# Performance work log

Measured on AMD Instinct MI355X. Metric: run time of the kernel, lower is better.

The kernel has to match this reference:

```python
import jax, jax.numpy as jnp
import numpy as np

C = 256
C8 = C // 8
B, H, W = 4, 64, 64


def setup_inputs() -> dict:
    key = jax.random.key(0)
    ks = jax.random.split(key, 10)
    s = lambda fan_in: 1.0 / np.sqrt(fan_in)
    return {
        "x": jax.random.normal(ks[0], (B, C, H, W), dtype=jnp.float32),
        "conv_w": jax.random.normal(ks[1], (C8, C), dtype=jnp.float32) * s(C),
        "conv_b": jax.random.normal(ks[2], (C8,), dtype=jnp.float32) * 0.01,
        "q_w": jax.random.normal(ks[3], (C8, C8), dtype=jnp.float32) * s(C8),
        "q_b": jax.random.normal(ks[4], (C8,), dtype=jnp.float32) * 0.01,
        "k_w": jax.random.normal(ks[5], (C8, C8), dtype=jnp.float32) * s(C8),
        "k_b": jax.random.normal(ks[6], (C8,), dtype=jnp.float32) * 0.01,
        "v_w": jax.random.normal(ks[7], (C, C8), dtype=jnp.float32) * s(C8),
        "v_b": jax.random.normal(ks[8], (C,), dtype=jnp.float32) * 0.01,
        "gamma": jax.random.normal(ks[9], (1,), dtype=jnp.float32) * 0.1,
    }


def reference(x, conv_w, conv_b, q_w, q_b, k_w, k_b, v_w, v_b, gamma):
    b, c, h, w = x.shape
    hw = h * w
    # 1x1 convs are channel-mixing matmuls over flattened spatial dims
    xf = x.reshape(b, c, hw)                                   # [B, C, HW]
    proj = jnp.einsum('dc,bcn->bdn', conv_w, xf) + conv_b[None, :, None]   # [B, C8, HW]
    q = jnp.einsum('ed,bdn->bne', q_w, proj) + q_b[None, None, :]          # [B, HW, C8]
    k = jnp.einsum('ed,bdn->ben', k_w, proj) + k_b[None, :, None]          # [B, C8, HW]
    v = jnp.einsum('cd,bdn->bcn', v_w, proj) + v_b[None, :, None]          # [B, C, HW]
    attn = jax.nn.softmax(jnp.einsum('bne,bem->bnm', q, k), axis=-1)       # [B, HW, HW]
    out = jnp.einsum('bcm,bnm->bcn', v, attn)                              # [B, C, HW]
    out = out.reshape(b, c, h, w)
    return gamma[0] * out + x
```

## Files before the change

### kernel.cpp

```cpp
#include <hip/hip_runtime.h>
#include <hip/hip_bf16.h>
#include <stdint.h>

#define B_   4
#define C_   256
#define C8_  32
#define HW_  4096
#define ROWS_ 320
#define MS_  4
#define L2E  1.4426950408889634f

typedef __attribute__((ext_vector_type(8)))  short  short8;
typedef __attribute__((ext_vector_type(8)))  ushort us8;
typedef __attribute__((ext_vector_type(16))) float  f32x16;

#define WT_OFF    0
#define BALL_OFF  (256*320*4)
#define Q_OFF     (BALL_OFF + 1280)
#define KT_OFF    (Q_OFF  + B_*HW_*C8_*2)
#define V_OFF     (KT_OFF + B_*HW_*C8_*2)
#define PACC_OFF  (V_OFF  + B_*C_*HW_*2)
#define LPART_OFF (PACC_OFF + (size_t)MS_*B_*C_*HW_*2)

__device__ __forceinline__ ushort f2bf(float f) {
    union { float f; uint32_t u; } v; v.f = f;
    uint32_t u = v.u;
    uint32_t r = u + 0x7fffu + ((u >> 16) & 1u);
    return (ushort)(r >> 16);
}
__device__ __forceinline__ uint32_t pktr(float lo, float hi) {
    union { float f; uint32_t u; } a, b; a.f = lo; b.f = hi;
    return __builtin_amdgcn_perm(b.u, a.u, 0x07060302u);
}

__global__ __launch_bounds__(256) void k_setup(
    const float* __restrict__ conv_w, const float* __restrict__ conv_b,
    const float* __restrict__ q_w, const float* __restrict__ q_b,
    const float* __restrict__ k_w, const float* __restrict__ k_b,
    const float* __restrict__ v_w, const float* __restrict__ v_b,
    ushort* __restrict__ wbf, float* __restrict__ ball)
{
    int r = blockIdx.x;
    int c = threadIdx.x;
    const float* wrow;
    float bias;
    if (r < 32)       { wrow = q_w + r*32;      bias = q_b[r];      }
    else if (r < 64)  { wrow = k_w + (r-32)*32; bias = k_b[r-32];   }
    else              { wrow = v_w + (r-64)*32; bias = v_b[r-64];   }
    float acc = 0.f;
    #pragma unroll
    for (int d = 0; d < 32; ++d) acc += wrow[d] * conv_w[d*C_ + c];
    float scale = (r < 32) ? L2E : 1.0f;
    wbf[r*C_ + c] = f2bf(acc * scale);
    if (c == 0) {
        float bb = bias;
        #pragma unroll
        for (int d = 0; d < 32; ++d) bb += wrow[d] * conv_b[d];
        ball[r] = bb * scale;
    }
}

__global__ __launch_bounds__(320) void k_qkv(
    const float* __restrict__ x, const ushort* __restrict__ wbf,
    const float* __restrict__ ball,
    ushort* __restrict__ qg, ushort* __restrict__ ktg, ushort* __restrict__ vg)
{
    int blk = blockIdx.x;
    int b  = blk >> 6;
    int n0 = (blk & 63) * 64;
    int t = threadIdx.x;
    int w = t >> 6, lane = t & 63;
    int l31 = lane & 31, h = lane >> 5;

    f32x16 acc[2][2];
    #pragma unroll
    for (int i = 0; i < 2; ++i)
        #pragma unroll
        for (int j = 0; j < 2; ++j)
            acc[i][j] = (f32x16)(0.f);

    const float* xb = x + (size_t)b*C_*HW_;
    const ushort* wrow0 = wbf + (size_t)(w*64 + l31)*C_ + h*8;
    const ushort* wrow1 = wrow0 + 32*C_;

    #pragma unroll 2
    for (int kc = 0; kc < 16; ++kc) {
        int k0 = kc*16;
        short8 a0 = *(const short8*)(wrow0 + k0);
        short8 a1 = *(const short8*)(wrow1 + k0);
        #pragma unroll
        for (int ni = 0; ni < 2; ++ni) {
            const float* xc = xb + (size_t)(k0 + h*8)*HW_ + n0 + ni*32 + l31;
            union { uint32_t d[4]; short8 s8; } bf;
            #pragma unroll
            for (int j2 = 0; j2 < 4; ++j2) {
                float f0 = xc[(size_t)(2*j2    )*HW_];
                float f1 = xc[(size_t)(2*j2 + 1)*HW_];
                bf.d[j2] = pktr(f0, f1);
            }
            acc[0][ni] = __builtin_amdgcn_mfma_f32_32x32x16_bf16(a0, bf.s8, acc[0][ni], 0, 0, 0);
            acc[1][ni] = __builtin_amdgcn_mfma_f32_32x32x16_bf16(a1, bf.s8, acc[1][ni], 0, 0, 0);
        }
    }

    #pragma unroll
    for (int mi = 0; mi < 2; ++mi) {
        int rowb = w*64 + mi*32;
        #pragma unroll
        for (int ni = 0; ni < 2; ++ni) {
            int n = n0 + ni*32 + l31;
            #pragma unroll
            for (int r = 0; r < 16; ++r) {
                int row = rowb + (r & 3) + 8*(r >> 2) + 4*h;
                float v = acc[mi][ni][r] + ball[row];
                ushort bv = f2bf(v);
                if (row < 32) {
                    qg[((size_t)b*HW_ + n)*C8_ + row] = bv;
                } else if (row < 64) {
                    ktg[((size_t)b*HW_ + n)*C8_ + (row - 32)] = bv;
                } else {
                    vg[((size_t)b*C_ + (row - 64))*HW_ + n] = bv;
                }
            }
        }
    }
}

__global__ __launch_bounds__(256, 2) void k_attn(
    const ushort* __restrict__ qg, const ushort* __restrict__ ktg,
    const ushort* __restrict__ vg,
    ushort* __restrict__ pacc, float* __restrict__ lpart)
{
    __shared__ ushort v_lds[2][16*512];
    __shared__ ushort kt_lds[2][4*512];

    int blk = blockIdx.x;
    int msid = blk & 3;
    int cs   = (blk >> 2) & 1;
    int qb   = (blk >> 3) & 15;
    int b    = blk >> 7;
    int t = threadIdx.x;
    int w = t >> 6, lane = t & 63;
    int l31 = lane & 31, h = lane >> 5;
    int qbase = qb*256 + w*64;
    int cbase = cs*128;
    int mbase = msid*1024;

    const ushort* kb_p = ktg + (size_t)b*HW_*C8_;
    const ushort* vb_p = vg  + (size_t)b*C_*HW_;

    short8 qf[2][2];
    #pragma unroll
    for (int qfr = 0; qfr < 2; ++qfr)
        #pragma unroll
        for (int ks = 0; ks < 2; ++ks)
            qf[qfr][ks] = *(const short8*)(qg + ((size_t)b*HW_ + qbase + qfr*32 + l31)*C8_
                                           + ks*16 + h*8);

    f32x16 acc[2][4];
    #pragma unroll
    for (int i = 0; i < 2; ++i)
        #pragma unroll
        for (int j = 0; j < 4; ++j)
            acc[i][j] = (f32x16)(0.f);
    float lsum[2] = {0.f, 0.f};

    #define STAGE(buf, m0)                                                          \
    {                                                                               \
        _Pragma("unroll")                                                           \
        for (int ks = 0; ks < 4; ++ks) {                                            \
            const ushort* src = vb_p + (size_t)(cbase + w*32 + l31)*HW_             \
                                + (m0) + ks*16 + h*8;                               \
            __builtin_amdgcn_global_load_lds(                                       \
                (const __attribute__((address_space(1))) uint32_t*)src,             \
                (__attribute__((address_space(3))) uint32_t*)&v_lds[buf][(w*4+ks)*512], \
                16, 0, 0);                                                          \
        }                                                                           \
        {                                                                           \
            int kb = w >> 1, ks = w & 1;                                            \
            const ushort* src = kb_p + (size_t)((m0) + kb*32 + l31)*C8_             \
                                + ks*16 + h*8;                                      \
            __builtin_amdgcn_global_load_lds(                                       \
                (const __attribute__((address_space(1))) uint32_t*)src,             \
                (__attribute__((address_space(3))) uint32_t*)&kt_lds[buf][w*512],   \
                16, 0, 0);                                                          \
        }                                                                           \
    }

    STAGE(0, mbase)
    __syncthreads();

    int buf = 0;
    for (int it = 0; it < 16; ++it) {
        if (it + 1 < 16) STAGE(buf ^ 1, mbase + (it+1)*64)

        short8 ktf[2][2];
        #pragma unroll
        for (int kb = 0; kb < 2; ++kb)
            #pragma unroll
            for (int ks = 0; ks < 2; ++ks)
                ktf[kb][ks] = *(const short8*)(&kt_lds[buf][(kb*2+ks)*512 + lane*8]);

        uint32_t up[4][8];
        #pragma unroll
        for (int qfr = 0; qfr < 2; ++qfr) {
            #pragma unroll
            for (int kb = 0; kb < 2; ++kb) {
                f32x16 s = (f32x16)(0.f);
                s = __builtin_amdgcn_mfma_f32_32x32x16_bf16(ktf[kb][0], qf[qfr][0], s, 0, 0, 0);
                s = __builtin_amdgcn_mfma_f32_32x32x16_bf16(ktf[kb][1], qf[qfr][1], s, 0, 0, 0);
                float e[16];
                #pragma unroll
                for (int r = 0; r < 16; ++r)
                    e[r] = __builtin_amdgcn_exp2f(s[r]);
                float2 tl2 = {0.f, 0.f};
                #pragma unroll
                for (int r = 0; r < 8; ++r) {
                    tl2.x += e[2*r];
                    tl2.y += e[2*r+1];
                }
                lsum[qfr] += tl2.x + tl2.y;
                #pragma unroll
                for (int i = 0; i < 8; ++i)
                    up[qfr*2+kb][i] = pktr(e[2*i], e[2*i+1]);
            }
        }

        short8 pf[2][4];
        #pragma unroll
        for (int qfr = 0; qfr < 2; ++qfr) {
            #pragma unroll
            for (int kb = 0; kb < 2; ++kb) {
                uint32_t* u = up[qfr*2+kb];
                uint32_t bpA = (uint32_t)__shfl_xor((int)(h ? u[0] : u[2]), 32);
                uint32_t bpB = (uint32_t)__shfl_xor((int)(h ? u[1] : u[3]), 32);
                uint32_t bpC = (uint32_t)__shfl_xor((int)(h ? u[4] : u[6]), 32);
                uint32_t bpD = (uint32_t)__shfl_xor((int)(h ? u[5] : u[7]), 32);
                union { uint32_t d[4]; short8 s8; } fe, fo;
                fe.d[0] = h ? bpA : u[0];  fe.d[1] = h ? bpB : u[1];
                fe.d[2] = h ? u[2] : bpA;  fe.d[3] = h ? u[3] : bpB;
                fo.d[0] = h ? bpC : u[4];  fo.d[1] = h ? bpD : u[5];
                fo.d[2] = h ? u[6] : bpC;  fo.d[3] = h ? u[7] : bpD;
                pf[qfr][kb*2 + 0] = fe.s8;
                pf[qfr][kb*2 + 1] = fo.s8;
            }
        }

        #pragma unroll
        for (int ks = 0; ks < 4; ++ks) {
            #pragma unroll
            for (int cfr = 0; cfr < 4; ++cfr) {
                short8 vf = *(const short8*)(&v_lds[buf][(cfr*4+ks)*512 + lane*8]);
                acc[0][cfr] = __builtin_amdgcn_mfma_f32_32x32x16_bf16(vf, pf[0][ks], acc[0][cfr], 0, 0, 0);
                acc[1][cfr] = __builtin_amdgcn_mfma_f32_32x32x16_bf16(vf, pf[1][ks], acc[1][cfr], 0, 0, 0);
            }
        }
        __syncthreads();
        buf ^= 1;
    }

    #pragma unroll
    for (int qfr = 0; qfr < 2; ++qfr) {
        union { float f; int i; } cv; cv.f = lsum[qfr];
        cv.i = __shfl_xor(cv.i, 32);
        lsum[qfr] += cv.f;
    }
    if (cs == 0 && h == 0) {
        #pragma unroll
        for (int qfr = 0; qfr < 2; ++qfr)
            lpart[(size_t)(msid*B_ + b)*HW_ + qbase + qfr*32 + l31] = lsum[qfr];
    }

    #pragma unroll
    for (int qfr = 0; qfr < 2; ++qfr) {
        int q = qbase + qfr*32 + l31;
        #pragma unroll
        for (int cfr = 0; cfr < 4; ++cfr) {
            #pragma unroll
            for (int r = 0; r < 16; ++r) {
                int c = cbase + cfr*32 + (r & 3) + 8*(r >> 2) + 4*h;
                pacc[((size_t)(msid*B_ + b)*C_ + c)*HW_ + q] = f2bf(acc[qfr][cfr][r]);
            }
        }
    }
    #undef STAGE
}

__global__ __launch_bounds__(256) void k_comb(
    const ushort* __restrict__ pacc, const float* __restrict__ lpart,
    const float* __restrict__ x, const float* __restrict__ gamma_p,
    float* __restrict__ out)
{
    int gid = blockIdx.x * 256 + threadIdx.x;
    int q8 = gid & 511;
    int c  = (gid >> 9) & 255;
    int b  = gid >> 17;
    size_t base = ((size_t)b*C_ + c)*HW_ + q8*8;

    float sum[8];
    #pragma unroll
    for (int k = 0; k < 8; ++k) sum[k] = 0.f;
    float lt[8];
    #pragma unroll
    for (int k = 0; k < 8; ++k) lt[k] = 0.f;

    #pragma unroll
    for (int ms = 0; ms < MS_; ++ms) {
        const ushort* pp = pacc + ((size_t)(ms*B_ + b)*C_ + c)*HW_ + q8*8;
        us8 v = *(const us8*)pp;
        #pragma unroll
        for (int k = 0; k < 8; ++k) {
            union { uint32_t u; float f; } cv; cv.u = ((uint32_t)v[k]) << 16;
            sum[k] += cv.f;
        }
        const float* lp = lpart + (size_t)(ms*B_ + b)*HW_ + q8*8;
        float4 l0 = *(const float4*)lp;
        float4 l1 = *(const float4*)(lp + 4);
        lt[0] += l0.x; lt[1] += l0.y; lt[2] += l0.z; lt[3] += l0.w;
        lt[4] += l1.x; lt[5] += l1.y; lt[6] += l1.z; lt[7] += l1.w;
    }

    float g = gamma_p[0];
    float4 x0 = *(const float4*)(x + base);
    float4 x1 = *(const float4*)(x + base + 4);
    float4 o0, o1;
    o0.x = g*sum[0]/lt[0] + x0.x;  o0.y = g*sum[1]/lt[1] + x0.y;
    o0.z = g*sum[2]/lt[2] + x0.z;  o0.w = g*sum[3]/lt[3] + x0.w;
    o1.x = g*sum[4]/lt[4] + x1.x;  o1.y = g*sum[5]/lt[5] + x1.y;
    o1.z = g*sum[6]/lt[6] + x1.z;  o1.w = g*sum[7]/lt[7] + x1.w;
    *(float4*)(out + base)     = o0;
    *(float4*)(out + base + 4) = o1;
}

extern "C" void kernel_launch(void* const* d_in, const int* in_sizes, int n_in,
                              void* d_out, int out_size, void* d_ws, size_t ws_size,
                              hipStream_t stream)
{
    const float* x      = (const float*)d_in[0];
    const float* conv_w = (const float*)d_in[1];
    const float* conv_b = (const float*)d_in[2];
    const float* q_w    = (const float*)d_in[3];
    const float* q_b    = (const float*)d_in[4];
    const float* k_w    = (const float*)d_in[5];
    const float* k_b    = (const float*)d_in[6];
    const float* v_w    = (const float*)d_in[7];
    const float* v_b    = (const float*)d_in[8];
    const float* gamma  = (const float*)d_in[9];
    float* out = (float*)d_out;

    char* ws = (char*)d_ws;
    ushort* wbf   = (ushort*)(ws + WT_OFF);
    float*  ball  = (float*)(ws + BALL_OFF);
    ushort* qg    = (ushort*)(ws + Q_OFF);
    ushort* ktg   = (ushort*)(ws + KT_OFF);
    ushort* vg    = (ushort*)(ws + V_OFF);
    ushort* pacc  = (ushort*)(ws + PACC_OFF);
    float*  lpart = (float*)(ws + LPART_OFF);

    k_setup<<<ROWS_, 256, 0, stream>>>(conv_w, conv_b, q_w, q_b, k_w, k_b,
                                       v_w, v_b, wbf, ball);
    k_qkv<<<B_*64, 320, 0, stream>>>(x, wbf, ball, qg, ktg, vg);
    k_attn<<<512, 256, 0, stream>>>(qg, ktg, vg, pacc, lpart);
    k_comb<<<(B_*C_*HW_/8 + 255)/256, 256, 0, stream>>>(pacc, lpart, x, gamma, out);
}
```

Measured before the change: 186.4 us.

## Use bit-trick exp2, retile attention loop, shrink qkv tiles, block pacc layout

After: 244.7 us. +31.3%, slower.

```diff
diff --git a/kernel.cpp b/kernel.cpp
--- a/kernel.cpp
+++ b/kernel.cpp
@@ -31,6 +31,12 @@
 __device__ __forceinline__ uint32_t pktr(float lo, float hi) {
     union { float f; uint32_t u; } a, b; a.f = lo; b.f = hi;
     return __builtin_amdgcn_perm(b.u, a.u, 0x07060302u);
+}
+__device__ __forceinline__ float fexp2(float s) {
+    float y = fmaf(s, 8388608.0f, 1064992506.0f);
+    y = fmaxf(y, 0.0f);
+    union { int i; float f; } c; c.i = (int)y;
+    return c.f;
 }
 
 __global__ __launch_bounds__(256) void k_setup(
@@ -66,61 +72,69 @@
     ushort* __restrict__ qg, ushort* __restrict__ ktg, ushort* __restrict__ vg)
 {
     int blk = blockIdx.x;
-    int b  = blk >> 6;
-    int n0 = (blk & 63) * 64;
+    int b  = blk >> 7;
+    int n0 = (blk & 127) * 32;
     int t = threadIdx.x;
     int w = t >> 6, lane = t & 63;
     int l31 = lane & 31, h = lane >> 5;
 
-    f32x16 acc[2][2];
-    #pragma unroll
-    for (int i = 0; i < 2; ++i)
-        #pragma unroll
-        for (int j = 0; j < 2; ++j)
-            acc[i][j] = (f32x16)(0.f);
-
-    const float* xb = x + (size_t)b*C_*HW_;
-    const ushort* wrow0 = wbf + (size_t)(w*64 + l31)*C_ + h*8;
-    const ushort* wrow1 = wrow0 + 32*C_;
+    f32x16 acc[2];
+    acc[0] = (f32x16)(0.f);
+    acc[1] = (f32x16)(0.f);
+
+    const float* xb = x + (size_t)b*C_*HW_ + n0 + l31;
+    const ushort* wr0 = wbf + (size_t)(w*64 + l31)*C_ + h*8;
+    const ushort* wr1 = wr0 + 32*C_;
 
     #pragma unroll 2
     for (int kc = 0; kc < 16; ++kc) {
         int k0 = kc*16;
-        short8 a0 = *(const short8*)(wrow0 + k0);
-        short8 a1 = *(const short8*)(wrow1 + k0);
-        #pragma unroll
-        for (int ni = 0; ni < 2; ++ni) {
-            const float* xc = xb + (size_t)(k0 + h*8)*HW_ + n0 + ni*32 + l31;
-            union { uint32_t d[4]; short8 s8; } bf;
-            #pragma unroll
-            for (int j2 = 0; j2 < 4; ++j2) {
-                float f0 = xc[(size_t)(2*j2    )*HW_];
-                float f1 = xc[(size_t)(2*j2 + 1)*HW_];
-                bf.d[j2] = pktr(f0, f1);
-            }
-            acc[0][ni] = __builtin_amdgcn_mfma_f32_32x32x16_bf16(a0, bf.s8, acc[0][ni], 0, 0, 0);
-            acc[1][ni] = __builtin_amdgcn_mfma_f32_32x32x16_bf16(a1, bf.s8, acc[1][ni], 0, 0, 0);
-        }
-    }
-
+        short8 a0 = *(const short8*)(wr0 + k0);
+        short8 a1 = *(const short8*)(wr1 + k0);
+        const float* xc = xb + (size_t)(k0 + h*8)*HW_;
+        union { uint32_t d[4]; short8 s8; } bf;
+        #pragma unroll
+        for (int j2 = 0; j2 < 4; ++j2) {
+            float f0 = xc[(size_t)(2*j2    )*HW_];
+            float f1 = xc[(size_t)(2*j2 + 1)*HW_];
+            bf.d[j2] = pktr(f0, f1);
+        }
+        acc[0] = __builtin_amdgcn_mfma_f32_32x32x16_bf16(a0, bf.s8, acc[0], 0, 0, 0);
+        acc[1] = __builtin_amdgcn_mfma_f32_32x32x16_bf16(a1, bf.s8, acc[1], 0, 0, 0);
+    }
+
+    int n = n0 + l31;
     #pragma unroll
     for (int mi = 0; mi < 2; ++mi) {
         int rowb = w*64 + mi*32;
-        #pragma unroll
-        for (int ni = 0; ni < 2; ++ni) {
-            int n = n0 + ni*32 + l31;
+        if (rowb == 0) {
+            #pragma unroll
+            for (int g = 0; g < 4; ++g) {
+                int r0 = g*8 + 4*h;
+                ushort4 pk;
+                pk.x = f2bf(acc[mi][g*4+0] + ball[r0+0]);
+                pk.y = f2bf(acc[mi][g*4+1] + ball[r0+1]);
+                pk.z = f2bf(acc[mi][g*4+2] + ball[r0+2]);
+                pk.w = f2bf(acc[mi][g*4+3] + ball[r0+3]);
+                *(ushort4*)(qg + ((size_t)b*HW_ + n)*C8_ + r0) = pk;
+            }
+        } else if (rowb == 32) {
+            #pragma unroll
+            for (int g = 0; g < 4; ++g) {
+                int e0 = g*8 + 4*h;
+                ushort4 pk;
+                pk.x = f2bf(acc[mi][g*4+0] + ball[32+e0+0]);
+                pk.y = f2bf(acc[mi][g*4+1] + ball[32+e0+1]);
+                pk.z = f2bf(acc[mi][g*4+2] + ball[32+e0+2]);
+                pk.w = f2bf(acc[mi][g*4+3] + ball[32+e0+3]);
+                *(ushort4*)(ktg + ((size_t)b*HW_ + n)*C8_ + e0) = pk;
+            }
+        } else {
             #pragma unroll
             for (int r = 0; r < 16; ++r) {
-                int row = rowb + (r & 3) + 8*(r >> 2) + 4*h;
-                float v = acc[mi][ni][r] + ball[row];
-                ushort bv = f2bf(v);
-                if (row < 32) {
-                    qg[((size_t)b*HW_ + n)*C8_ + row] = bv;
-                } else if (row < 64) {
-                    ktg[((size_t)b*HW_ + n)*C8_ + (row - 32)] = bv;
-                } else {
-                    vg[((size_t)b*C_ + (row - 64))*HW_ + n] = bv;
-                }
+                int roff = (r & 3) + 8*(r >> 2) + 4*h;
+                int c = rowb - 64 + roff;
+                vg[((size_t)b*C_ + c)*HW_ + n] = f2bf(acc[mi][r] + ball[rowb + roff]);
             }
         }
     }
@@ -131,23 +145,22 @@
     const ushort* __restrict__ vg,
     ushort* __restrict__ pacc, float* __restrict__ lpart)
 {
-    __shared__ ushort v_lds[2][16*512];
-    __shared__ ushort kt_lds[2][4*512];
+    __shared__ ushort v_lds[32*512];
+    __shared__ ushort kt_lds[8*512];
 
     int blk = blockIdx.x;
-    int msid = blk & 3;
-    int cs   = (blk >> 2) & 1;
-    int qb   = (blk >> 3) & 15;
-    int b    = blk >> 7;
+    int qb = blk & 15;
+    int cs = (blk >> 4) & 1;
+    int ms = (blk >> 5) & 3;
+    int b  = blk >> 7;
     int t = threadIdx.x;
     int w = t >> 6, lane = t & 63;
     int l31 = lane & 31, h = lane >> 5;
     int qbase = qb*256 + w*64;
-    int cbase = cs*128;
-    int mbase = msid*1024;
+    int mbase = ms*1024;
 
     const ushort* kb_p = ktg + (size_t)b*HW_*C8_;
-    const ushort* vb_p = vg  + (size_t)b*C_*HW_;
+    const ushort* vb_p = vg  + (size_t)b*C_*HW_ + (size_t)(cs*128 + w*32 + l31)*HW_;
 
     short8 qf[2][2];
     #pragma unroll
@@ -165,73 +178,53 @@
             acc[i][j] = (f32x16)(0.f);
     float lsum[2] = {0.f, 0.f};
 
-    #define STAGE(buf, m0)                                                          \
-    {                                                                               \
-        _Pragma("unroll")                                                           \
-        for (int ks = 0; ks < 4; ++ks) {                                            \
-            const ushort* src = vb_p + (size_t)(cbase + w*32 + l31)*HW_             \
-                                + (m0) + ks*16 + h*8;                               \
-            __builtin_amdgcn_global_load_lds(                                       \
-                (const __attribute__((address_space(1))) uint32_t*)src,             \
-                (__attribute__((address_space(3))) uint32_t*)&v_lds[buf][(w*4+ks)*512], \
-                16, 0, 0);                                                          \
-        }                                                                           \
-        {                                                                           \
-            int kb = w >> 1, ks = w & 1;                                            \
-            const ushort* src = kb_p + (size_t)((m0) + kb*32 + l31)*C8_             \
-                                + ks*16 + h*8;                                      \
-            __builtin_amdgcn_global_load_lds(                                       \
-                (const __attribute__((address_space(1))) uint32_t*)src,             \
-                (__attribute__((address_space(3))) uint32_t*)&kt_lds[buf][w*512],   \
-                16, 0, 0);                                                          \
-        }                                                                           \
-    }
-
-    STAGE(0, mbase)
-    __syncthreads();
-
-    int buf = 0;
-    for (int it = 0; it < 16; ++it) {
-        if (it + 1 < 16) STAGE(buf ^ 1, mbase + (it+1)*64)
-
-        short8 ktf[2][2];
-        #pragma unroll
-        for (int kb = 0; kb < 2; ++kb)
-            #pragma unroll
-            for (int ks = 0; ks < 2; ++ks)
-                ktf[kb][ks] = *(const short8*)(&kt_lds[buf][(kb*2+ks)*512 + lane*8]);
-
-        uint32_t up[4][8];
-        #pragma unroll
-        for (int qfr = 0; qfr < 2; ++qfr) {
-            #pragma unroll
-            for (int kb = 0; kb < 2; ++kb) {
+    for (int it = 0; it < 8; ++it) {
+        int m0 = mbase + it*128;
+        __syncthreads();
+        #pragma unroll
+        for (int ks = 0; ks < 8; ++ks) {
+            const ushort* src = vb_p + m0 + ks*16 + h*8;
+            __builtin_amdgcn_global_load_lds(
+                (const __attribute__((address_space(1))) uint32_t*)src,
+                (__attribute__((address_space(3))) uint32_t*)&v_lds[(w*8+ks)*512],
+                16, 0, 0);
+        }
+        #pragma unroll
+        for (int j = 0; j < 2; ++j) {
+            const ushort* src = kb_p + (size_t)(m0 + w*32 + l31)*C8_ + j*16 + h*8;
+            __builtin_amdgcn_global_load_lds(
+                (const __attribute__((address_space(1))) uint32_t*)src,
+                (__attribute__((address_space(3))) uint32_t*)&kt_lds[(w*2+j)*512],
+                16, 0, 0);
+        }
+        __syncthreads();
+
+        #pragma unroll
+        for (int kb = 0; kb < 4; ++kb) {
+            short8 kt0 = *(const short8*)(&kt_lds[(kb*2+0)*512 + lane*8]);
+            short8 kt1 = *(const short8*)(&kt_lds[(kb*2+1)*512 + lane*8]);
+
+            uint32_t up[2][8];
+            #pragma unroll
+            for (int qfr = 0; qfr < 2; ++qfr) {
                 f32x16 s = (f32x16)(0.f);
-                s = __builtin_amdgcn_mfma_f32_32x32x16_bf16(ktf[kb][0], qf[qfr][0], s, 0, 0, 0);
-                s = __builtin_amdgcn_mfma_f32_32x32x16_bf16(ktf[kb][1], qf[qfr][1], s, 0, 0, 0);
+                s = __builtin_amdgcn_mfma_f32_32x32x16_bf16(kt0, qf[qfr][0], s, 0, 0, 0);
+                s = __builtin_amdgcn_mfma_f32_32x32x16_bf16(kt1, qf[qfr][1], s, 0, 0, 0);
                 float e[16];
                 #pragma unroll
-                for (int r = 0; r < 16; ++r)
-                    e[r] = __builtin_amdgcn_exp2f(s[r]);
-                float2 tl2 = {0.f, 0.f};
+                for (int r = 0; r < 16; ++r) e[r] = fexp2(s[r]);
+                float t0 = 0.f, t1 = 0.f;
                 #pragma unroll
-                for (int r = 0; r < 8; ++r) {
-                    tl2.x += e[2*r];
-                    tl2.y += e[2*r+1];
-                }
-                lsum[qfr] += tl2.x + tl2.y;
+                for (int r = 0; r < 8; ++r) { t0 += e[2*r]; t1 += e[2*r+1]; }
+                lsum[qfr] += t0 + t1;
                 #pragma unroll
-                for (int i = 0; i < 8; ++i)
-                    up[qfr*2+kb][i] = pktr(e[2*i], e[2*i+1]);
-            }
-        }
-
-        short8 pf[2][4];
-        #pragma unroll
-        for (int qfr = 0; qfr < 2; ++qfr) {
-            #pragma unroll
-            for (int kb = 0; kb < 2; ++kb) {
-                uint32_t* u = up[qfr*2+kb];
+                for (int i = 0; i < 8; ++i) up[qfr][i] = pktr(e[2*i], e[2*i+1]);
+            }
+
+            short8 pf[2][2];
+            #pragma unroll
+            for (int qfr = 0; qfr < 2; ++qfr) {
+                uint32_t* u = up[qfr];
                 uint32_t bpA = (uint32_t)__shfl_xor((int)(h ? u[0] : u[2]), 32);
                 uint32_t bpB = (uint32_t)__shfl_xor((int)(h ? u[1] : u[3]), 32);
                 uint32_t bpC = (uint32_t)__shfl_xor((int)(h ? u[4] : u[6]), 32);
@@ -241,22 +234,21 @@
                 fe.d[2] = h ? u[2] : bpA;  fe.d[3] = h ? u[3] : bpB;
                 fo.d[0] = h ? bpC : u[4];  fo.d[1] = h ? bpD : u[5];
                 fo.d[2] = h ? u[6] : bpC;  fo.d[3] = h ? u[7] : bpD;
-                pf[qfr][kb*2 + 0] = fe.s8;
-                pf[qfr][kb*2 + 1] = fo.s8;
-            }
-        }
-
-        #pragma unroll
-        for (int ks = 0; ks < 4; ++ks) {
-            #pragma unroll
-            for (int cfr = 0; cfr < 4; ++cfr) {
-                short8 vf = *(const short8*)(&v_lds[buf][(cfr*4+ks)*512 + lane*8]);
-                acc[0][cfr] = __builtin_amdgcn_mfma_f32_32x32x16_bf16(vf, pf[0][ks], acc[0][cfr], 0, 0, 0);
-                acc[1][cfr] = __builtin_amdgcn_mfma_f32_32x32x16_bf16(vf, pf[1][ks], acc[1][cfr], 0, 0, 0);
-            }
-        }
-        __syncthreads();
-        buf ^= 1;
+                pf[qfr][0] = fe.s8;
+                pf[qfr][1] = fo.s8;
+            }
+
+            #pragma unroll
+            for (int ksub = 0; ksub < 2; ++ksub) {
+                int ks = kb*2 + ksub;
+                #pragma unroll
+                for (int cfr = 0; cfr < 4; ++cfr) {
+                    short8 vf = *(const short8*)(&v_lds[(cfr*8 + ks)*512 + lane*8]);
+                    acc[0][cfr] = __builtin_amdgcn_mfma_f32_32x32x16_bf16(vf, pf[0][ksub], acc[0][cfr], 0, 0, 0);
+                    acc[1][cfr] = __builtin_amdgcn_mfma_f32_32x32x16_bf16(vf, pf[1][ksub], acc[1][cfr], 0, 0, 0);
+                }
+            }
+        }
     }
 
     #pragma unroll
@@ -268,22 +260,22 @@
     if (cs == 0 && h == 0) {
         #pragma unroll
         for (int qfr = 0; qfr < 2; ++qfr)
-            lpart[(size_t)(msid*B_ + b)*HW_ + qbase + qfr*32 + l31] = lsum[qfr];
-    }
-
+            lpart[(size_t)(ms*B_ + b)*HW_ + qbase + qfr*32 + l31] = lsum[qfr];
+    }
+
+    size_t pbase = ((size_t)(ms*B_ + b)*16 + qb);
     #pragma unroll
     for (int qfr = 0; qfr < 2; ++qfr) {
-        int q = qbase + qfr*32 + l31;
+        int ql = w*64 + qfr*32 + l31;
         #pragma unroll
         for (int cfr = 0; cfr < 4; ++cfr) {
             #pragma unroll
             for (int r = 0; r < 16; ++r) {
-                int c = cbase + cfr*32 + (r & 3) + 8*(r >> 2) + 4*h;
-                pacc[((size_t)(msid*B_ + b)*C_ + c)*HW_ + q] = f2bf(acc[qfr][cfr][r]);
-            }
-        }
-    }
-    #undef STAGE
+                int c = cs*128 + cfr*32 + (r & 3) + 8*(r >> 2) + 4*h;
+                pacc[((pbase*C_ + c) << 8) + ql] = f2bf(acc[qfr][cfr][r]);
+            }
+        }
+    }
 }
 
 __global__ __launch_bounds__(256) void k_comb(
@@ -295,7 +287,9 @@
     int q8 = gid & 511;
     int c  = (gid >> 9) & 255;
     int b  = gid >> 17;
-    size_t base = ((size_t)b*C_ + c)*HW_ + q8*8;
+    int q  = q8 * 8;
+    int qt = q >> 8, qq = q & 255;
+    size_t base = ((size_t)b*C_ + c)*HW_ + q;
 
     float sum[8];
     #pragma unroll
@@ -306,14 +300,14 @@
 
     #pragma unroll
     for (int ms = 0; ms < MS_; ++ms) {
-        const ushort* pp = pacc + ((size_t)(ms*B_ + b)*C_ + c)*HW_ + q8*8;
+        const ushort* pp = pacc + ((((size_t)(ms*B_ + b)*16 + qt)*C_ + c) << 8) + qq;
         us8 v = *(const us8*)pp;
         #pragma unroll
         for (int k = 0; k < 8; ++k) {
             union { uint32_t u; float f; } cv; cv.u = ((uint32_t)v[k]) << 16;
             sum[k] += cv.f;
         }
-        const float* lp = lpart + (size_t)(ms*B_ + b)*HW_ + q8*8;
+        const float* lp = lpart + (size_t)(ms*B_ + b)*HW_ + q;
         float4 l0 = *(const float4*)lp;
         float4 l1 = *(const float4*)(lp + 4);
         lt[0] += l0.x; lt[1] += l0.y; lt[2] += l0.z; lt[3] += l0.w;
@@ -359,7 +353,7 @@
 
     k_setup<<<ROWS_, 256, 0, stream>>>(conv_w, conv_b, q_w, q_b, k_w, k_b,
                                        v_w, v_b, wbf, ball);
-    k_qkv<<<B_*64, 320, 0, stream>>>(x, wbf, ball, qg, ktg, vg);
+    k_qkv<<<B_*128, 320, 0, stream>>>(x, wbf, ball, qg, ktg, vg);
     k_attn<<<512, 256, 0, stream>>>(qg, ktg, vg, pacc, lpart);
     k_comb<<<(B_*C_*HW_/8 + 255)/256, 256, 0, stream>>>(pacc, lpart, x, gamma, out);
 }
```
